# Optimization experiments

Measured on AMD Instinct MI355X. Metric: run time of the kernel, lower is better.

Reference implementation:

```python
import jax, jax.numpy as jnp
import numpy as np

B, T, M, C, H = 2, 2048, 512, 512, 8
D = C // H
SCALE = 1.0 / np.sqrt(D).astype(np.float32)


def _linear_params(key, din, dout):
    kw, kb = jax.random.split(key)
    W = jax.random.normal(kw, (din, dout), jnp.float32) * 0.02
    b = jax.random.normal(kb, (dout,), jnp.float32) * 0.02
    return W, b


def setup_inputs() -> dict:
    key = jax.random.key(0)
    ks = jax.random.split(key, 8)
    x = jax.random.normal(ks[0], (B, T, C), jnp.float32)
    y = jax.random.normal(ks[1], (B, M, C), jnp.float32)
    # causal mask over the x (self / product-attn) axis, broadcasts to [B,H,T,T]
    attn_x_mask = jnp.tril(jnp.ones((T, T), jnp.int32))[None, None]
    Wqkv_x, bqkv_x = _linear_params(ks[2], C, 3 * C)
    Wqkv_y, bqkv_y = _linear_params(ks[3], C, 3 * C)
    Wgs, bgs = _linear_params(ks[4], C, C)
    Wgc, bgc = _linear_params(ks[5], C, C)
    Wp, bp = _linear_params(ks[6], C, C)
    return dict(x=x, y=y, attn_x_mask=attn_x_mask,
                Wqkv_x=Wqkv_x, bqkv_x=bqkv_x, Wqkv_y=Wqkv_y, bqkv_y=bqkv_y,
                Wgs=Wgs, bgs=bgs, Wgc=Wgc, bgc=bgc, Wp=Wp, bp=bp)


def _heads(t, L):
    # [B,L,C] -> [B,H,L,D]
    return t.reshape(B, L, H, D).transpose(0, 2, 1, 3)


def reference(x, y, attn_x_mask, Wqkv_x, bqkv_x, Wqkv_y, bqkv_y,
              Wgs, bgs, Wgc, bgc, Wp, bp):
    neg_inf = jnp.float32(-jnp.inf)
    qx, kx, vx = jnp.split(x @ Wqkv_x + bqkv_x, 3, axis=-1)
    qy, ky, vy = jnp.split(y @ Wqkv_y + bqkv_y, 3, axis=-1)
    q_x, k_x, v_x = _heads(qx, T), _heads(kx, T), _heads(vx, T)
    q_y, k_y, v_y = _heads(qy, M), _heads(ky, M), _heads(vy, M)

    # cross attention x -> y : [B,H,T,M]
    catt_x2y = jnp.einsum('bhtd,bhmd->bhtm', q_x, k_y) * SCALE
    cval_x2y = jnp.einsum('bhtm,bhmd->bhtd', jax.nn.softmax(catt_x2y, axis=-1), v_y)
    cval_x2y = cval_x2y.transpose(0, 2, 1, 3).reshape(B, T, C)

    # product attention: (x->y scores) @ (y->x scores) : [B,H,T,T]
    catt_y2x = jnp.einsum('bhmd,bhtd->bhmt', q_y, k_x) * SCALE
    prod = jnp.einsum('bhtm,bhms->bhts', catt_x2y, catt_y2x) * SCALE
    prod = jnp.where(attn_x_mask == 0, neg_inf, prod)
    cval_y2x = jnp.einsum('bhts,bhsd->bhtd', jax.nn.softmax(prod, axis=-1), v_x)
    cval_y2x = cval_y2x.transpose(0, 2, 1, 3).reshape(B, T, C)

    cval = cval_x2y + cval_y2x

    # self attention on x : [B,H,T,T]
    satt = jnp.einsum('bhtd,bhsd->bhts', q_x, k_x) * SCALE
    satt = jnp.where(attn_x_mask == 0, neg_inf, satt)
    sval = jnp.einsum('bhts,bhsd->bhtd', jax.nn.softmax(satt, axis=-1), v_x)
    sval = sval.transpose(0, 2, 1, 3).reshape(B, T, C)

    sgate = jax.nn.sigmoid(sval @ Wgs + bgs)
    cgate = jax.nn.sigmoid(cval @ Wgc + bgc)
    out = (sgate * cval + cgate * sval) @ Wp + bp
    return out
```

## Files before the change

### kernel.cpp

```cpp
#include <hip/hip_runtime.h>
#include <hip/hip_bf16.h>

typedef unsigned short ushort_t;
typedef __attribute__((ext_vector_type(8))) short s8v;
typedef __attribute__((ext_vector_type(4))) float f4;
typedef __attribute__((ext_vector_type(4))) unsigned short u16x4;

#define BB 2
#define TT 2048
#define MMM 512
#define CC 512
#define HH 8
#define DD 64
#define SCALE 0.125f
#define SCALE_L2E 0.18033688011112042f

__device__ __forceinline__ ushort_t f2bf(float v) {
    __hip_bfloat16 h = __float2bfloat16(v);
    return *reinterpret_cast<ushort_t*>(&h);
}
__device__ __forceinline__ float bf2f(ushort_t u) {
    __hip_bfloat16 h;
    *reinterpret_cast<ushort_t*>(&h) = u;
    return __bfloat162float(h);
}
__device__ __forceinline__ float exp2_raw(float v) {
    float p;
    asm("v_exp_f32 %0, %1" : "=v"(p) : "v"(v));
    return p;
}

__device__ __forceinline__ void gload16(const void* g, void* l) {
    __builtin_amdgcn_global_load_lds((const __attribute__((address_space(1))) void*)g,
                                     (__attribute__((address_space(3))) void*)l, 16, 0, 0);
}

__device__ __forceinline__ void transp32(const float* W, ushort_t* WT, int K, int N,
                                         int bx, int by, int tid) {
    const int k0 = by * 32, n0 = bx * 32;
    __shared__ float t[32][33];
    for (int i = tid; i < 1024; i += 256) {
        int r = i >> 5, c = i & 31;
        t[r][c] = W[(long)(k0 + r) * N + n0 + c];
    }
    __syncthreads();
    for (int i = tid; i < 1024; i += 256) {
        int r = i >> 5, c = i & 31;
        WT[(long)(n0 + r) * K + k0 + c] = f2bf(t[c][r]);
    }
}
__device__ __forceinline__ void cvt4(const float* s, ushort_t* d, long blk, int tid) {
    long i = (blk * 256 + tid) * 4;
    float4 v = *(const float4*)(s + i);
    u16x4 o;
    o[0] = f2bf(v.x); o[1] = f2bf(v.y); o[2] = f2bf(v.z); o[3] = f2bf(v.w);
    *(u16x4*)(d + i) = o;
}

__global__ __launch_bounds__(256) void prep_k(
    const float* __restrict__ x, const float* __restrict__ y,
    const float* __restrict__ Wqx, const float* __restrict__ Wqy,
    const float* __restrict__ Wgs, const float* __restrict__ Wgc,
    const float* __restrict__ Wp,
    ushort_t* __restrict__ xb, ushort_t* __restrict__ yb,
    ushort_t* __restrict__ WqxT, ushort_t* __restrict__ WqyT,
    ushort_t* __restrict__ WgsT, ushort_t* __restrict__ WgcT,
    ushort_t* __restrict__ WpT)
{
    const int bid = blockIdx.x, tid = threadIdx.x;
    if (bid < 2048)      cvt4(x, xb, bid, tid);
    else if (bid < 2560) cvt4(y, yb, bid - 2048, tid);
    else if (bid < 3328) { int l = bid - 2560; transp32(Wqx, WqxT, 512, 1536, l % 48, l / 48, tid); }
    else if (bid < 4096) { int l = bid - 3328; transp32(Wqy, WqyT, 512, 1536, l % 48, l / 48, tid); }
    else if (bid < 4352) { int l = bid - 4096; transp32(Wgs, WgsT, 512, 512, l % 16, l / 16, tid); }
    else if (bid < 4608) { int l = bid - 4352; transp32(Wgc, WgcT, 512, 512, l % 16, l / 16, tid); }
    else                 { int l = bid - 4608; transp32(Wp, WpT, 512, 512, l % 16, l / 16, tid); }
}

__global__ __launch_bounds__(256) void vT_fused(
    const ushort_t* __restrict__ qkvx, const ushort_t* __restrict__ qkvy,
    ushort_t* __restrict__ vxT, ushort_t* __restrict__ vyT,
    ushort_t* __restrict__ kyT, ushort_t* __restrict__ qyT)
{
    const int bx = blockIdx.x, z = blockIdx.y, b = z >> 3, h = z & 7;
    const ushort_t* src; ushort_t* dst; int S, s0; long sB, dZ;
    if (bx < 32)      { src = qkvx + 1024; dst = vxT; S = TT;  sB = (long)TT * 1536;  dZ = (long)64 * TT;  s0 = bx * 64; }
    else if (bx < 40) { src = qkvy + 1024; dst = vyT; S = MMM; sB = (long)MMM * 1536; dZ = (long)64 * MMM; s0 = (bx - 32) * 64; }
    else if (bx < 48) { src = qkvy + 512;  dst = kyT; S = MMM; sB = (long)MMM * 1536; dZ = (long)64 * MMM; s0 = (bx - 40) * 64; }
    else              { src = qkvy;        dst = qyT; S = MMM; sB = (long)MMM * 1536; dZ = (long)64 * MMM; s0 = (bx - 48) * 64; }
    const ushort_t* sp = src + (long)b * sB + (long)h * 64;
    ushort_t* dp = dst + (long)z * dZ;
    __shared__ __align__(16) ushort_t t[64][80];
    const int tid = threadIdx.x;
#pragma unroll
    for (int p = 0; p < 2; ++p) {
        int id = tid + p * 256;
        int r = id >> 3, cc = (id & 7) * 8;
        int cs = cc ^ ((r >> 3) * 8);
        *(s8v*)&t[r][cs] = *(const s8v*)&sp[(long)(s0 + r) * 1536 + cc];
    }
    __syncthreads();
#pragma unroll
    for (int p = 0; p < 2; ++p) {
        int id = tid + p * 256;
        int d = id >> 3, cc = (id & 7) * 8;
        s8v o;
#pragma unroll
        for (int k = 0; k < 8; ++k) {
            int r = cc + k;
            o[k] = (short)t[r][d ^ ((r >> 3) * 8)];
        }
        *(s8v*)&dp[(long)d * S + s0 + cc] = o;
    }
}

__device__ __forceinline__ void stage_rows128(const ushort_t* src, long k0,
                                              ushort_t* dstL, int w, int lane) {
#pragma unroll
    for (int n = 0; n < 4; ++n) {
        int f = w * 4096 + n * 1024 + lane * 16;
        int row = f >> 7;
        int blk_g = ((f & 127) >> 4) ^ (row & 7);
        gload16(src + (long)row * 512 + k0 + blk_g * 8, dstL + ((w * 4096 + n * 1024) >> 1));
    }
}
__device__ __forceinline__ void stage_rows64(const ushort_t* src, long k0,
                                             ushort_t* dstL, int w, int lane) {
#pragma unroll
    for (int n = 0; n < 2; ++n) {
        int f = w * 2048 + n * 1024 + lane * 16;
        int row = f >> 7;
        int blk_g = ((f & 127) >> 4) ^ (row & 7);
        gload16(src + (long)row * 512 + k0 + blk_g * 8, dstL + ((w * 2048 + n * 1024) >> 1));
    }
}

__global__ __launch_bounds__(256) void qkv_k(
    const ushort_t* __restrict__ xb, const ushort_t* __restrict__ yb,
    const ushort_t* __restrict__ WqxT, const ushort_t* __restrict__ WqyT,
    const float* __restrict__ bqx, const float* __restrict__ bqy,
    ushort_t* __restrict__ qkvx, ushort_t* __restrict__ qkvy)
{
    const int by = blockIdx.y;
    const ushort_t* A; const ushort_t* Bm; const float* bias; ushort_t* O;
    int r0, qcols;
    if (by < 32) { A = xb; Bm = WqxT; bias = bqx; O = qkvx; r0 = by * 128; qcols = 512; }
    else         { A = yb; Bm = WqyT; bias = bqy; O = qkvy; r0 = (by - 32) * 128; qcols = 0; }
    const int c0 = blockIdx.x * 128;
    const int tid = threadIdx.x, w = tid >> 6, lane = tid & 63;
    const int quad = lane >> 4, l15 = lane & 15;
    const int rowBase = (w >> 1) * 64, colBase = (w & 1) * 64;

    __shared__ __align__(16) ushort_t Al[2][128 * 64];
    __shared__ __align__(16) ushort_t Bl[2][128 * 64];

    const ushort_t* Ab = A + (long)r0 * 512;
    const ushort_t* Bb = Bm + (long)c0 * 512;

    f4 acc[4][4] = {};

    stage_rows128(Ab, 0, Al[0], w, lane);
    stage_rows128(Bb, 0, Bl[0], w, lane);
    __syncthreads();

    for (int kk = 0; kk < 8; ++kk) {
        const int cur = kk & 1;
        if (kk < 7) {
            stage_rows128(Ab, (kk + 1) * 64, Al[cur ^ 1], w, lane);
            stage_rows128(Bb, (kk + 1) * 64, Bl[cur ^ 1], w, lane);
        }
#pragma unroll
        for (int ks = 0; ks < 2; ++ks) {
            s8v af[4], bfr[4];
#pragma unroll
            for (int i = 0; i < 4; ++i) {
                int row = rowBase + 16 * i + l15;
                af[i] = *(const s8v*)&Al[cur][row * 64 + (((ks * 4 + quad) ^ (row & 7)) * 8)];
                int col = colBase + 16 * i + l15;
                bfr[i] = *(const s8v*)&Bl[cur][col * 64 + (((ks * 4 + quad) ^ (col & 7)) * 8)];
            }
#pragma unroll
            for (int i = 0; i < 4; ++i)
#pragma unroll
                for (int j = 0; j < 4; ++j)
                    acc[i][j] = __builtin_amdgcn_mfma_f32_16x16x32_bf16(af[i], bfr[j], acc[i][j], 0, 0, 0);
        }
        __syncthreads();
    }

#pragma unroll
    for (int i = 0; i < 4; ++i)
#pragma unroll
        for (int j = 0; j < 4; ++j)
#pragma unroll
            for (int r = 0; r < 4; ++r) {
                int row = r0 + rowBase + 16 * i + quad * 4 + r;
                int col = c0 + colBase + 16 * j + l15;
                float v = acc[i][j][r] + bias[col];
                if (col < qcols) v *= SCALE_L2E;
                O[(long)row * 1536 + col] = f2bf(v);
            }
}

__global__ __launch_bounds__(256) void proj_k(
    const ushort_t* __restrict__ A, const ushort_t* __restrict__ Bm,
    float* __restrict__ O, const float* __restrict__ bias)
{
    const int r0 = blockIdx.y * 64, c0 = blockIdx.x * 64;
    const int tid = threadIdx.x, w = tid >> 6, lane = tid & 63;
    const int quad = lane >> 4, l15 = lane & 15;
    const int rowBase = (w >> 1) * 32, colBase = (w & 1) * 32;

    __shared__ __align__(16) ushort_t Al[3][64 * 64];
    __shared__ __align__(16) ushort_t Bl[3][64 * 64];

    const ushort_t* Ab = A + (long)r0 * 512;
    const ushort_t* Bb = Bm + (long)c0 * 512;

    f4 acc[2][2] = {};

    stage_rows64(Ab, 0, Al[0], w, lane);
    stage_rows64(Bb, 0, Bl[0], w, lane);
    stage_rows64(Ab, 64, Al[1], w, lane);
    stage_rows64(Bb, 64, Bl[1], w, lane);

    int cur = 0;
    for (int kk = 0; kk < 8; ++kk) {
        if (kk + 1 < 8) asm volatile("s_waitcnt vmcnt(4)" ::: "memory");
        else            asm volatile("s_waitcnt vmcnt(0)" ::: "memory");
        asm volatile("s_barrier" ::: "memory");
        if (kk + 2 < 8) {
            int s = cur + 2; if (s >= 3) s -= 3;
            stage_rows64(Ab, (kk + 2) * 64, Al[s], w, lane);
            stage_rows64(Bb, (kk + 2) * 64, Bl[s], w, lane);
        }
#pragma unroll
        for (int ks = 0; ks < 2; ++ks) {
            s8v af[2], bfr[2];
#pragma unroll
            for (int i = 0; i < 2; ++i) {
                int row = rowBase + 16 * i + l15;
                af[i] = *(const s8v*)&Al[cur][row * 64 + (((ks * 4 + quad) ^ (row & 7)) * 8)];
                int col = colBase + 16 * i + l15;
                bfr[i] = *(const s8v*)&Bl[cur][col * 64 + (((ks * 4 + quad) ^ (col & 7)) * 8)];
            }
#pragma unroll
            for (int i = 0; i < 2; ++i)
#pragma unroll
                for (int j = 0; j < 2; ++j)
                    acc[i][j] = __builtin_amdgcn_mfma_f32_16x16x32_bf16(af[i], bfr[j], acc[i][j], 0, 0, 0);
        }
        if (++cur == 3) cur = 0;
    }

#pragma unroll
    for (int i = 0; i < 2; ++i)
#pragma unroll
        for (int j = 0; j < 2; ++j)
#pragma unroll
            for (int r = 0; r < 4; ++r) {
                int row = r0 + rowBase + 16 * i + quad * 4 + r;
                int col = c0 + colBase + 16 * j + l15;
                O[(long)row * 512 + col] = acc[i][j][r] + bias[col];
            }
}

__global__ __launch_bounds__(256) void gt_k(const ushort_t* __restrict__ qyT,
                                            const ushort_t* __restrict__ kyT,
                                            ushort_t* __restrict__ Gt)
{
    const int z = blockIdx.x;
    const int tid = threadIdx.x, w = tid >> 6, lane = tid & 63;
    const int quad = lane >> 4, l15 = lane & 15;
    const ushort_t* A  = qyT + (long)z * 64 * MMM;
    const ushort_t* Bm = kyT + (long)z * 64 * MMM;
    __shared__ float red[4][4096];
    f4 acc[4][4] = {};
    for (int kk = 0; kk < 4; ++kk) {
        const int ks = w * 4 + kk;
        s8v af[4], bfr[4];
#pragma unroll
        for (int i = 0; i < 4; ++i) {
            af[i]  = *(const s8v*)(A  + (long)(16 * i + l15) * MMM + ks * 32 + quad * 8);
            bfr[i] = *(const s8v*)(Bm + (long)(16 * i + l15) * MMM + ks * 32 + quad * 8);
        }
#pragma unroll
        for (int i = 0; i < 4; ++i)
#pragma unroll
            for (int j = 0; j < 4; ++j)
                acc[i][j] = __builtin_amdgcn_mfma_f32_16x16x32_bf16(af[i], bfr[j], acc[i][j], 0, 0, 0);
    }
#pragma unroll
    for (int i = 0; i < 4; ++i)
#pragma unroll
        for (int j = 0; j < 4; ++j)
            *(f4*)&red[w][(i * 4 + j) * 256 + lane * 4] = acc[i][j];
    __syncthreads();
    const float s2 = SCALE * SCALE;
#pragma unroll
    for (int j = 0; j < 4; ++j) {
        f4 s = *(const f4*)&red[0][(w * 4 + j) * 256 + lane * 4];
#pragma unroll
        for (int ww = 1; ww < 4; ++ww)
            s += *(const f4*)&red[ww][(w * 4 + j) * 256 + lane * 4];
#pragma unroll
        for (int r = 0; r < 4; ++r) {
            int d2 = 16 * w + quad * 4 + r, d1 = 16 * j + l15;
            Gt[(long)z * 4096 + d2 * 64 + d1] = f2bf(s2 * s[r]);
        }
    }
}

__device__ __forceinline__ void stage_k64(const ushort_t* src, long rstride, int s0,
                                          ushort_t* Kl, int w, int lane) {
#pragma unroll
    for (int n = 0; n < 2; ++n) {
        int f = w * 2048 + n * 1024 + lane * 16;
        int row = f >> 7;
        int krow = ((row & 15) << 2) | (row >> 4);
        int blk = ((f & 127) >> 4) ^ (row & 7);
        gload16(src + (long)(s0 + krow) * rstride + blk * 8, &Kl[(w * 2048 + n * 1024) >> 1]);
    }
}
__device__ __forceinline__ void stage_v64(const ushort_t* src, long rstride, int s0,
                                          ushort_t* Vl, int w, int lane) {
#pragma unroll
    for (int n = 0; n < 2; ++n) {
        int f = w * 2048 + n * 1024 + lane * 16;
        int row = f >> 7;
        int blk = ((f & 127) >> 4) ^ (row & 7);
        gload16(src + (long)row * rstride + s0 + blk * 8, &Vl[(w * 2048 + n * 1024) >> 1]);
    }
}
__device__ __forceinline__ void qk8(f4 Sc[4], const s8v qf[2], const ushort_t* Kl,
                                    int quad, int l15) {
    __builtin_amdgcn_s_setprio(1);
#pragma unroll
    for (int ks = 0; ks < 2; ++ks)
#pragma unroll
        for (int c = 0; c < 4; ++c) {
            int row = 16 * c + l15;
            s8v bb = *(const s8v*)&Kl[row * 64 + (((ks * 4 + quad) ^ (row & 7)) * 8)];
            Sc[c] = __builtin_amdgcn_mfma_f32_16x16x32_bf16(qf[ks], bb, Sc[c], 0, 0, 0);
        }
    __builtin_amdgcn_s_setprio(0);
}
__device__ __forceinline__ void qk8_dual(f4 Ss[4], f4 Sp[4], const s8v qa[2], const s8v qb[2],
                                         const ushort_t* Kl, int quad, int l15) {
    __builtin_amdgcn_s_setprio(1);
#pragma unroll
    for (int ks = 0; ks < 2; ++ks)
#pragma unroll
        for (int c = 0; c < 4; ++c) {
            int row = 16 * c + l15;
            s8v bb = *(const s8v*)&Kl[row * 64 + (((ks * 4 + quad) ^ (row & 7)) * 8)];
            Ss[c] = __builtin_amdgcn_mfma_f32_16x16x32_bf16(qa[ks], bb, Ss[c], 0, 0, 0);
            Sp[c] = __builtin_amdgcn_mfma_f32_16x16x32_bf16(qb[ks], bb, Sp[c], 0, 0, 0);
        }
    __builtin_amdgcn_s_setprio(0);
}
__device__ __forceinline__ void vload8(s8v vf[8], const ushort_t* Vl, int quad, int l15) {
#pragma unroll
    for (int ks = 0; ks < 2; ++ks)
#pragma unroll
        for (int c = 0; c < 4; ++c) {
            int row = 16 * c + l15;
            vf[ks * 4 + c] = *(const s8v*)&Vl[row * 64 + (((ks * 4 + quad) ^ (row & 7)) * 8)];
        }
}
__device__ __forceinline__ void smax0(const f4 Sc[4], float l_i[4], ushort_t* PlW,
                                      int diag, int trow0, int s0, int quad, int l15) {
#pragma unroll
    for (int r = 0; r < 4; ++r) {
        const int trow = trow0 + quad * 4 + r;
        u16x4 o;
#pragma unroll
        for (int c = 0; c < 4; ++c) {
            float v = Sc[c][r];
            if (diag && (s0 + 4 * l15 + c) > trow) v = -3e38f;
            float p = exp2_raw(v);
            l_i[r] += p;
            o[c] = f2bf(p);
        }
        *(u16x4*)&PlW[(quad * 4 + r) * 72 + 4 * l15] = o;
    }
}
__device__ __forceinline__ void pv8r(f4 Oc[4], const ushort_t* PlW, const s8v vf[8],
                                     int quad, int l15) {
    __builtin_amdgcn_s_setprio(1);
#pragma unroll
    for (int ks = 0; ks < 2; ++ks) {
        s8v a = *(const s8v*)&PlW[l15 * 72 + ks * 32 + quad * 8];
#pragma unroll
        for (int c = 0; c < 4; ++c)
            Oc[c] = __builtin_amdgcn_mfma_f32_16x16x32_bf16(a, vf[ks * 4 + c], Oc[c], 0, 0, 0);
    }
    __builtin_amdgcn_s_setprio(0);
}
__device__ __forceinline__ void pv8r_dual(f4 Os[4], f4 Op[4], const ushort_t* Ps,
                                          const ushort_t* Pp, const s8v vf[8],
                                          int quad, int l15) {
    __builtin_amdgcn_s_setprio(1);
#pragma unroll
    for (int ks = 0; ks < 2; ++ks) {
        s8v as = *(const s8v*)&Ps[l15 * 72 + ks * 32 + quad * 8];
        s8v ap = *(const s8v*)&Pp[l15 * 72 + ks * 32 + quad * 8];
#pragma unroll
        for (int c = 0; c < 4; ++c) {
            Os[c] = __builtin_amdgcn_mfma_f32_16x16x32_bf16(as, vf[ks * 4 + c], Os[c], 0, 0, 0);
            Op[c] = __builtin_amdgcn_mfma_f32_16x16x32_bf16(ap, vf[ks * 4 + c], Op[c], 0, 0, 0);
        }
    }
    __builtin_amdgcn_s_setprio(0);
}

__global__ __launch_bounds__(256, 2) void flash_fused(
    const ushort_t* __restrict__ qkvx, const ushort_t* __restrict__ qkvy,
    const ushort_t* __restrict__ Gt, const ushort_t* __restrict__ vxT,
    const ushort_t* __restrict__ vyT,
    ushort_t* __restrict__ cval, ushort_t* __restrict__ sval)
{
    const int z = blockIdx.y, b = z >> 3, h = z & 7;
    const ushort_t* qx = qkvx + (long)b * (TT * 1536) + h * 64;
    const ushort_t* kx = qx + 512;
    const ushort_t* ky = qkvy + (long)b * (MMM * 1536) + 512 + h * 64;
    const ushort_t* Gz = Gt + (long)z * 4096;
    const ushort_t* vx = vxT + (long)z * (64 * TT);
    const ushort_t* vy = vyT + (long)z * (64 * MMM);

    const int xw = (z & 8) ? (int)blockIdx.x : (int)(gridDim.x - 1 - blockIdx.x);
    const int t0 = xw * 64;
    const int tid = threadIdx.x, w = tid >> 6, lane = tid & 63;
    const int quad = lane >> 4, l15 = lane & 15;

    __shared__ __align__(16) ushort_t Kl[2][64 * 64];
    __shared__ __align__(16) ushort_t Vl[2][64 * 64];
    __shared__ __align__(16) ushort_t Pl[2][4 * 16 * 72];
    ushort_t* PlWs = &Pl[0][w * 1152];
    ushort_t* PlWp = &Pl[1][w * 1152];

    stage_k64(ky, 1536, 0, Kl[0], w, lane);
    stage_v64(vy, MMM, 0, Vl[0], w, lane);

    const int qrow = t0 + 16 * w + l15;
    s8v qfx[2], qft[2];
    qfx[0] = *(const s8v*)(qx + (long)qrow * 1536 + quad * 8);
    qfx[1] = *(const s8v*)(qx + (long)qrow * 1536 + 32 + quad * 8);
    {
        f4 qa[4] = {};
#pragma unroll
        for (int ks = 0; ks < 2; ++ks)
#pragma unroll
            for (int j = 0; j < 4; ++j) {
                s8v bb = *(const s8v*)(Gz + (4 * l15 + j) * 64 + ks * 32 + quad * 8);
                qa[j] = __builtin_amdgcn_mfma_f32_16x16x32_bf16(qfx[ks], bb, qa[j], 0, 0, 0);
            }
#pragma unroll
        for (int r = 0; r < 4; ++r) {
            u16x4 o;
#pragma unroll
            for (int j = 0; j < 4; ++j) o[j] = f2bf(qa[j][r]);
            *(u16x4*)&PlWs[(quad * 4 + r) * 72 + 4 * l15] = o;
        }
        qft[0] = *(const s8v*)&PlWs[l15 * 72 + quad * 8];
        qft[1] = *(const s8v*)&PlWs[l15 * 72 + 32 + quad * 8];
    }

    f4 Occ[4] = {}, Ocs[4] = {}, Ocp[4] = {};
    float lc[4] = {}, ls[4] = {}, lp[4] = {};

    const int nT1 = MMM / 64;
    const int nTiles = nT1 + t0 / 64 + 1;

    for (int ti = 0; ti < nTiles; ++ti) {
        const int bi = ti & 1;
        __syncthreads();
        if (ti + 1 < nTiles) {
            const int tn = ti + 1, bn = tn & 1;
            if (tn < nT1) {
                stage_k64(ky, 1536, tn * 64, Kl[bn], w, lane);
                stage_v64(vy, MMM, tn * 64, Vl[bn], w, lane);
            } else {
                const int s0n = (tn - nT1) * 64;
                stage_k64(kx, 1536, s0n, Kl[bn], w, lane);
                stage_v64(vx, TT, s0n, Vl[bn], w, lane);
            }
        }
        if (ti < nT1) {
            f4 Sc[4] = {};
            qk8(Sc, qfx, Kl[bi], quad, l15);
            s8v vf[8];
            vload8(vf, Vl[bi], quad, l15);
            smax0(Sc, lc, PlWs, 0, 0, 0, quad, l15);
            pv8r(Occ, PlWs, vf, quad, l15);
        } else {
            const int s0 = (ti - nT1) * 64;
            const int diag = (s0 == t0);
            f4 Ss[4] = {}, Sp[4] = {};
            qk8_dual(Ss, Sp, qfx, qft, Kl[bi], quad, l15);
            s8v vf[8];
            vload8(vf, Vl[bi], quad, l15);
            smax0(Ss, ls, PlWs, diag, t0 + 16 * w, s0, quad, l15);
            smax0(Sp, lp, PlWp, diag, t0 + 16 * w, s0, quad, l15);
            pv8r_dual(Ocs, Ocp, PlWs, PlWp, vf, quad, l15);
        }
    }

#pragma unroll
    for (int r = 0; r < 4; ++r)
#pragma unroll
        for (int mb = 1; mb < 16; mb <<= 1) {
            lc[r] += __shfl_xor(lc[r], mb, 64);
            ls[r] += __shfl_xor(ls[r], mb, 64);
            lp[r] += __shfl_xor(lp[r], mb, 64);
        }

    const long ob = (long)b * (TT * CC) + h * 64;
#pragma unroll
    for (int r = 0; r < 4; ++r) {
        int row = t0 + 16 * w + quad * 4 + r;
        float ic = 1.f / lc[r], ip = 1.f / lp[r], isv = 1.f / ls[r];
#pragma unroll
        for (int c = 0; c < 4; ++c) {
            long idx = ob + (long)row * CC + 16 * c + l15;
            cval[idx] = f2bf(Occ[c][r] * ic + Ocp[c][r] * ip);
            sval[idx] = f2bf(Ocs[c][r] * isv);
        }
    }
}

__global__ __launch_bounds__(256) void gate_gemm(
    const ushort_t* __restrict__ sval, const ushort_t* __restrict__ cvalb,
    const ushort_t* __restrict__ WgsT, const ushort_t* __restrict__ WgcT,
    const float* __restrict__ bgs, const float* __restrict__ bgc,
    ushort_t* __restrict__ tmpb)
{
    const int r0 = blockIdx.y * 64, c0 = blockIdx.x * 64;
    const int tid = threadIdx.x, w = tid >> 6, lane = tid & 63;
    const int quad = lane >> 4, l15 = lane & 15;
    const int rowBase = (w >> 1) * 32, colBase = (w & 1) * 32;

    __shared__ __align__(16) ushort_t Al[3][64 * 64];
    __shared__ __align__(16) ushort_t Bl[3][64 * 64];

    const ushort_t* Ap[2] = { sval + (long)r0 * 512, cvalb + (long)r0 * 512 };
    const ushort_t* Bp[2] = { WgsT + (long)c0 * 512, WgcT + (long)c0 * 512 };

    f4 acc1[2][2] = {}, acc2[2][2] = {};

    stage_rows64(Ap[0], 0, Al[0], w, lane);
    stage_rows64(Bp[0], 0, Bl[0], w, lane);
    stage_rows64(Ap[0], 64, Al[1], w, lane);
    stage_rows64(Bp[0], 64, Bl[1], w, lane);

    int cur = 0;
    for (int st = 0; st < 16; ++st) {
        if (st + 1 < 16) asm volatile("s_waitcnt vmcnt(4)" ::: "memory");
        else             asm volatile("s_waitcnt vmcnt(0)" ::: "memory");
        asm volatile("s_barrier" ::: "memory");
        if (st + 2 < 16) {
            int s = cur + 2; if (s >= 3) s -= 3;
            const int nx = st + 2, p = nx >> 3;
            stage_rows64(Ap[p], (nx & 7) * 64, Al[s], w, lane);
            stage_rows64(Bp[p], (nx & 7) * 64, Bl[s], w, lane);
        }
#pragma unroll
        for (int ks = 0; ks < 2; ++ks) {
            s8v af[2], bfr[2];
#pragma unroll
            for (int i = 0; i < 2; ++i) {
                int row = rowBase + 16 * i + l15;
                af[i] = *(const s8v*)&Al[cur][row * 64 + (((ks * 4 + quad) ^ (row & 7)) * 8)];
                int col = colBase + 16 * i + l15;
                bfr[i] = *(const s8v*)&Bl[cur][col * 64 + (((ks * 4 + quad) ^ (col & 7)) * 8)];
            }
            if (st < 8) {
#pragma unroll
                for (int i = 0; i < 2; ++i)
#pragma unroll
                    for (int j = 0; j < 2; ++j)
                        acc1[i][j] = __builtin_amdgcn_mfma_f32_16x16x32_bf16(af[i], bfr[j], acc1[i][j], 0, 0, 0);
            } else {
#pragma unroll
                for (int i = 0; i < 2; ++i)
#pragma unroll
                    for (int j = 0; j < 2; ++j)
                        acc2[i][j] = __builtin_amdgcn_mfma_f32_16x16x32_bf16(af[i], bfr[j], acc2[i][j], 0, 0, 0);
            }
        }
        if (++cur == 3) cur = 0;
    }

#pragma unroll
    for (int i = 0; i < 2; ++i)
#pragma unroll
        for (int j = 0; j < 2; ++j)
#pragma unroll
            for (int r = 0; r < 4; ++r) {
                int row = r0 + rowBase + 16 * i + quad * 4 + r;
                int col = c0 + colBase + 16 * j + l15;
                long idx = (long)row * 512 + col;
                float g1 = 1.f / (1.f + __expf(-(acc1[i][j][r] + bgs[col])));
                float g2 = 1.f / (1.f + __expf(-(acc2[i][j][r] + bgc[col])));
                tmpb[idx] = f2bf(g1 * bf2f(cvalb[idx]) + g2 * bf2f(sval[idx]));
            }
}

extern "C" void kernel_launch(void* const* d_in, const int* in_sizes, int n_in,
                              void* d_out, int out_size, void* d_ws, size_t ws_size,
                              hipStream_t stream) {
    const float* x      = (const float*)d_in[0];
    const float* y      = (const float*)d_in[1];
    const float* Wqkv_x = (const float*)d_in[3];
    const float* bqkv_x = (const float*)d_in[4];
    const float* Wqkv_y = (const float*)d_in[5];
    const float* bqkv_y = (const float*)d_in[6];
    const float* Wgs    = (const float*)d_in[7];
    const float* bgs    = (const float*)d_in[8];
    const float* Wgc    = (const float*)d_in[9];
    const float* bgc    = (const float*)d_in[10];
    const float* Wp     = (const float*)d_in[11];
    const float* bp     = (const float*)d_in[12];
    float* out = (float*)d_out;

    ushort_t* u = (ushort_t*)d_ws;
    long o = 0;
    ushort_t* xb    = u + o; o += (long)BB * TT * CC;
    ushort_t* yb    = u + o; o += (long)BB * MMM * CC;
    ushort_t* WqxT  = u + o; o += 1536L * 512;
    ushort_t* WqyT  = u + o; o += 1536L * 512;
    ushort_t* WgsT  = u + o; o += 512L * 512;
    ushort_t* WgcT  = u + o; o += 512L * 512;
    ushort_t* WpT   = u + o; o += 512L * 512;
    ushort_t* qkvx  = u + o; o += (long)BB * TT * 1536;
    ushort_t* qkvy  = u + o; o += (long)BB * MMM * 1536;
    ushort_t* vxT   = u + o; o += (long)BB * HH * DD * TT;
    ushort_t* vyT   = u + o; o += (long)BB * HH * DD * MMM;
    ushort_t* kyT   = u + o; o += (long)BB * HH * DD * MMM;
    ushort_t* qyT   = u + o; o += (long)BB * HH * DD * MMM;
    ushort_t* Gt    = u + o; o += 16L * 64 * 64;
    ushort_t* cvalb = u + o; o += (long)BB * TT * CC;
    ushort_t* sval  = u + o; o += (long)BB * TT * CC;
    ushort_t* tmpb  = u + o; o += (long)BB * TT * CC;

    dim3 blk(256);

    prep_k<<<dim3(4864), blk, 0, stream>>>(x, y, Wqkv_x, Wqkv_y, Wgs, Wgc, Wp,
                                           xb, yb, WqxT, WqyT, WgsT, WgcT, WpT);

    qkv_k<<<dim3(12, 40), blk, 0, stream>>>(xb, yb, WqxT, WqyT, bqkv_x, bqkv_y, qkvx, qkvy);

    vT_fused<<<dim3(56, 16), blk, 0, stream>>>(qkvx, qkvy, vxT, vyT, kyT, qyT);

    gt_k<<<dim3(16), blk, 0, stream>>>(qyT, kyT, Gt);

    flash_fused<<<dim3(32, 16), blk, 0, stream>>>(qkvx, qkvy, Gt, vxT, vyT, cvalb, sval);

    gate_gemm<<<dim3(8, 64), blk, 0, stream>>>(sval, cvalb, WgsT, WgcT, bgs, bgc, tmpb);

    proj_k<<<dim3(8, 64), blk, 0, stream>>>(tmpb, WpT, out, bp);
}
```

Measured before the change: 205.8 us.

## Keep softmax probabilities in registers by computing transposed scores in flash kernel

Swaps the MFMA operands in the QK step so each lane holds a score column whose layout matches the A-operand of a 16x16x16 bf16 MFMA. The P@V product then uses the probabilities directly from registers, which removes the per-wave LDS round trip for P and the Pl shared buffer. V is read in 4-element chunks to match the new layout, the K staging row permutation is dropped, and row sums are reduced and broadcast with shuffles. The trade-off is twice as many smaller MFMAs for P@V, and correctness now depends on the new masking index math and the Kl[1] scratch reuse.

Result: no change. 209.2 us (+1.7%).

```diff
diff --git a/kernel.cpp b/kernel.cpp
--- a/kernel.cpp
+++ b/kernel.cpp
@@ -3,6 +3,7 @@
 
 typedef unsigned short ushort_t;
 typedef __attribute__((ext_vector_type(8))) short s8v;
+typedef __attribute__((ext_vector_type(4))) short s4v;
 typedef __attribute__((ext_vector_type(4))) float f4;
 typedef __attribute__((ext_vector_type(4))) unsigned short u16x4;
 
@@ -28,6 +29,21 @@
     float p;
     asm("v_exp_f32 %0, %1" : "=v"(p) : "v"(v));
     return p;
+}
+
+#if defined(__has_builtin)
+#if __has_builtin(__builtin_amdgcn_mfma_f32_16x16x16bf16_1k)
+#define HAVE_MFMA16 1
+#endif
+#endif
+__device__ __forceinline__ f4 mfma16(s4v a, s4v b, f4 c) {
+#ifdef HAVE_MFMA16
+    return __builtin_amdgcn_mfma_f32_16x16x16bf16_1k(a, b, c, 0, 0, 0);
+#else
+    s8v a8 = {a[0], a[1], a[2], a[3], 0, 0, 0, 0};
+    s8v b8 = {b[0], b[1], b[2], b[3], 0, 0, 0, 0};
+    return __builtin_amdgcn_mfma_f32_16x16x32_bf16(a8, b8, c, 0, 0, 0);
+#endif
 }
 
 __device__ __forceinline__ void gload16(const void* g, void* l) {
@@ -317,9 +333,8 @@
     for (int n = 0; n < 2; ++n) {
         int f = w * 2048 + n * 1024 + lane * 16;
         int row = f >> 7;
-        int krow = ((row & 15) << 2) | (row >> 4);
         int blk = ((f & 127) >> 4) ^ (row & 7);
-        gload16(src + (long)(s0 + krow) * rstride + blk * 8, &Kl[(w * 2048 + n * 1024) >> 1]);
+        gload16(src + (long)(s0 + row) * rstride + blk * 8, &Kl[(w * 2048 + n * 1024) >> 1]);
     }
 }
 __device__ __forceinline__ void stage_v64(const ushort_t* src, long rstride, int s0,
@@ -332,85 +347,78 @@
         gload16(src + (long)row * rstride + s0 + blk * 8, &Vl[(w * 2048 + n * 1024) >> 1]);
     }
 }
-__device__ __forceinline__ void qk8(f4 Sc[4], const s8v qf[2], const ushort_t* Kl,
-                                    int quad, int l15) {
+__device__ __forceinline__ void qk8_sw(f4 Sc[4], const s8v qf[2], const ushort_t* Kl,
+                                       int quad, int l15) {
     __builtin_amdgcn_s_setprio(1);
 #pragma unroll
     for (int ks = 0; ks < 2; ++ks)
 #pragma unroll
         for (int c = 0; c < 4; ++c) {
             int row = 16 * c + l15;
-            s8v bb = *(const s8v*)&Kl[row * 64 + (((ks * 4 + quad) ^ (row & 7)) * 8)];
-            Sc[c] = __builtin_amdgcn_mfma_f32_16x16x32_bf16(qf[ks], bb, Sc[c], 0, 0, 0);
+            s8v kk = *(const s8v*)&Kl[row * 64 + (((ks * 4 + quad) ^ (row & 7)) * 8)];
+            Sc[c] = __builtin_amdgcn_mfma_f32_16x16x32_bf16(kk, qf[ks], Sc[c], 0, 0, 0);
         }
     __builtin_amdgcn_s_setprio(0);
 }
-__device__ __forceinline__ void qk8_dual(f4 Ss[4], f4 Sp[4], const s8v qa[2], const s8v qb[2],
-                                         const ushort_t* Kl, int quad, int l15) {
+__device__ __forceinline__ void qk8_dual_sw(f4 Ss[4], f4 Sp[4], const s8v qa[2], const s8v qb[2],
+                                            const ushort_t* Kl, int quad, int l15) {
     __builtin_amdgcn_s_setprio(1);
 #pragma unroll
     for (int ks = 0; ks < 2; ++ks)
 #pragma unroll
         for (int c = 0; c < 4; ++c) {
             int row = 16 * c + l15;
-            s8v bb = *(const s8v*)&Kl[row * 64 + (((ks * 4 + quad) ^ (row & 7)) * 8)];
-            Ss[c] = __builtin_amdgcn_mfma_f32_16x16x32_bf16(qa[ks], bb, Ss[c], 0, 0, 0);
-            Sp[c] = __builtin_amdgcn_mfma_f32_16x16x32_bf16(qb[ks], bb, Sp[c], 0, 0, 0);
+            s8v kk = *(const s8v*)&Kl[row * 64 + (((ks * 4 + quad) ^ (row & 7)) * 8)];
+            Ss[c] = __builtin_amdgcn_mfma_f32_16x16x32_bf16(kk, qa[ks], Ss[c], 0, 0, 0);
+            Sp[c] = __builtin_amdgcn_mfma_f32_16x16x32_bf16(kk, qb[ks], Sp[c], 0, 0, 0);
         }
     __builtin_amdgcn_s_setprio(0);
 }
-__device__ __forceinline__ void vload8(s8v vf[8], const ushort_t* Vl, int quad, int l15) {
-#pragma unroll
-    for (int ks = 0; ks < 2; ++ks)
-#pragma unroll
-        for (int c = 0; c < 4; ++c) {
-            int row = 16 * c + l15;
-            vf[ks * 4 + c] = *(const s8v*)&Vl[row * 64 + (((ks * 4 + quad) ^ (row & 7)) * 8)];
-        }
-}
-__device__ __forceinline__ void smax0(const f4 Sc[4], float l_i[4], ushort_t* PlW,
-                                      int diag, int trow0, int s0, int quad, int l15) {
-#pragma unroll
-    for (int r = 0; r < 4; ++r) {
-        const int trow = trow0 + quad * 4 + r;
-        u16x4 o;
-#pragma unroll
-        for (int c = 0; c < 4; ++c) {
+__device__ __forceinline__ void vload16(s4v vb[16], const ushort_t* Vl, int quad, int l15) {
+#pragma unroll
+    for (int c = 0; c < 4; ++c)
+#pragma unroll
+        for (int td = 0; td < 4; ++td) {
+            int row = 16 * td + l15;
+            int blk = (2 * c + (quad >> 1)) ^ (row & 7);
+            vb[c * 4 + td] = *(const s4v*)&Vl[row * 64 + blk * 8 + (quad & 1) * 4];
+        }
+}
+__device__ __forceinline__ void smax_pack(const f4 Sc[4], float& l_acc, s4v pa[4],
+                                          int diag, int trow, int s0, int quad) {
+#pragma unroll
+    for (int c = 0; c < 4; ++c) {
+        s4v o;
+#pragma unroll
+        for (int r = 0; r < 4; ++r) {
             float v = Sc[c][r];
-            if (diag && (s0 + 4 * l15 + c) > trow) v = -3e38f;
+            if (diag && (s0 + 16 * c + 4 * quad + r) > trow) v = -3e38f;
             float p = exp2_raw(v);
-            l_i[r] += p;
-            o[c] = f2bf(p);
-        }
-        *(u16x4*)&PlW[(quad * 4 + r) * 72 + 4 * l15] = o;
-    }
-}
-__device__ __forceinline__ void pv8r(f4 Oc[4], const ushort_t* PlW, const s8v vf[8],
-                                     int quad, int l15) {
+            l_acc += p;
+            o[r] = (short)f2bf(p);
+        }
+        pa[c] = o;
+    }
+}
+__device__ __forceinline__ void pv16(f4 Oc[4], const s4v pa[4], const s4v vb[16]) {
     __builtin_amdgcn_s_setprio(1);
 #pragma unroll
-    for (int ks = 0; ks < 2; ++ks) {
-        s8v a = *(const s8v*)&PlW[l15 * 72 + ks * 32 + quad * 8];
-#pragma unroll
-        for (int c = 0; c < 4; ++c)
-            Oc[c] = __builtin_amdgcn_mfma_f32_16x16x32_bf16(a, vf[ks * 4 + c], Oc[c], 0, 0, 0);
-    }
+    for (int c = 0; c < 4; ++c)
+#pragma unroll
+        for (int td = 0; td < 4; ++td)
+            Oc[td] = mfma16(pa[c], vb[c * 4 + td], Oc[td]);
     __builtin_amdgcn_s_setprio(0);
 }
-__device__ __forceinline__ void pv8r_dual(f4 Os[4], f4 Op[4], const ushort_t* Ps,
-                                          const ushort_t* Pp, const s8v vf[8],
-                                          int quad, int l15) {
+__device__ __forceinline__ void pv16_dual(f4 Os[4], f4 Op[4], const s4v pas[4],
+                                          const s4v pap[4], const s4v vb[16]) {
     __builtin_amdgcn_s_setprio(1);
 #pragma unroll
-    for (int ks = 0; ks < 2; ++ks) {
-        s8v as = *(const s8v*)&Ps[l15 * 72 + ks * 32 + quad * 8];
-        s8v ap = *(const s8v*)&Pp[l15 * 72 + ks * 32 + quad * 8];
-#pragma unroll
-        for (int c = 0; c < 4; ++c) {
-            Os[c] = __builtin_amdgcn_mfma_f32_16x16x32_bf16(as, vf[ks * 4 + c], Os[c], 0, 0, 0);
-            Op[c] = __builtin_amdgcn_mfma_f32_16x16x32_bf16(ap, vf[ks * 4 + c], Op[c], 0, 0, 0);
-        }
-    }
+    for (int c = 0; c < 4; ++c)
+#pragma unroll
+        for (int td = 0; td < 4; ++td) {
+            Os[td] = mfma16(pas[c], vb[c * 4 + td], Os[td]);
+            Op[td] = mfma16(pap[c], vb[c * 4 + td], Op[td]);
+        }
     __builtin_amdgcn_s_setprio(0);
 }
 
@@ -432,12 +440,10 @@
     const int t0 = xw * 64;
     const int tid = threadIdx.x, w = tid >> 6, lane = tid & 63;
     const int quad = lane >> 4, l15 = lane & 15;
+    const int trow = t0 + 16 * w + l15;
 
     __shared__ __align__(16) ushort_t Kl[2][64 * 64];
     __shared__ __align__(16) ushort_t Vl[2][64 * 64];
-    __shared__ __align__(16) ushort_t Pl[2][4 * 16 * 72];
-    ushort_t* PlWs = &Pl[0][w * 1152];
-    ushort_t* PlWp = &Pl[1][w * 1152];
 
     stage_k64(ky, 1536, 0, Kl[0], w, lane);
     stage_v64(vy, MMM, 0, Vl[0], w, lane);
@@ -455,19 +461,20 @@
                 s8v bb = *(const s8v*)(Gz + (4 * l15 + j) * 64 + ks * 32 + quad * 8);
                 qa[j] = __builtin_amdgcn_mfma_f32_16x16x32_bf16(qfx[ks], bb, qa[j], 0, 0, 0);
             }
+        ushort_t* scr = &Kl[1][w * 1024];
 #pragma unroll
         for (int r = 0; r < 4; ++r) {
             u16x4 o;
 #pragma unroll
             for (int j = 0; j < 4; ++j) o[j] = f2bf(qa[j][r]);
-            *(u16x4*)&PlWs[(quad * 4 + r) * 72 + 4 * l15] = o;
-        }
-        qft[0] = *(const s8v*)&PlWs[l15 * 72 + quad * 8];
-        qft[1] = *(const s8v*)&PlWs[l15 * 72 + 32 + quad * 8];
+            *(u16x4*)&scr[(quad * 4 + r) * 64 + 4 * l15] = o;
+        }
+        qft[0] = *(const s8v*)&scr[l15 * 64 + quad * 8];
+        qft[1] = *(const s8v*)&scr[l15 * 64 + 32 + quad * 8];
     }
 
     f4 Occ[4] = {}, Ocs[4] = {}, Ocp[4] = {};
-    float lc[4] = {}, ls[4] = {}, lp[4] = {};
+    float lc = 0.f, ls = 0.f, lp = 0.f;
 
     const int nT1 = MMM / 64;
     const int nTiles = nT1 + t0 / 64 + 1;
@@ -488,43 +495,42 @@
         }
         if (ti < nT1) {
             f4 Sc[4] = {};
-            qk8(Sc, qfx, Kl[bi], quad, l15);
-            s8v vf[8];
-            vload8(vf, Vl[bi], quad, l15);
-            smax0(Sc, lc, PlWs, 0, 0, 0, quad, l15);
-            pv8r(Occ, PlWs, vf, quad, l15);
+            qk8_sw(Sc, qfx, Kl[bi], quad, l15);
+            s4v vb[16];
+            vload16(vb, Vl[bi], quad, l15);
+            s4v pa[4];
+            smax_pack(Sc, lc, pa, 0, 0, 0, quad);
+            pv16(Occ, pa, vb);
         } else {
             const int s0 = (ti - nT1) * 64;
             const int diag = (s0 == t0);
             f4 Ss[4] = {}, Sp[4] = {};
-            qk8_dual(Ss, Sp, qfx, qft, Kl[bi], quad, l15);
-            s8v vf[8];
-            vload8(vf, Vl[bi], quad, l15);
-            smax0(Ss, ls, PlWs, diag, t0 + 16 * w, s0, quad, l15);
-            smax0(Sp, lp, PlWp, diag, t0 + 16 * w, s0, quad, l15);
-            pv8r_dual(Ocs, Ocp, PlWs, PlWp, vf, quad, l15);
-        }
-    }
-
-#pragma unroll
-    for (int r = 0; r < 4; ++r)
-#pragma unroll
-        for (int mb = 1; mb < 16; mb <<= 1) {
-            lc[r] += __shfl_xor(lc[r], mb, 64);
-            ls[r] += __shfl_xor(ls[r], mb, 64);
-            lp[r] += __shfl_xor(lp[r], mb, 64);
-        }
+            qk8_dual_sw(Ss, Sp, qfx, qft, Kl[bi], quad, l15);
+            s4v vb[16];
+            vload16(vb, Vl[bi], quad, l15);
+            s4v pas[4], pap[4];
+            smax_pack(Ss, ls, pas, diag, trow, s0, quad);
+            smax_pack(Sp, lp, pap, diag, trow, s0, quad);
+            pv16_dual(Ocs, Ocp, pas, pap, vb);
+        }
+    }
+
+    lc += __shfl_xor(lc, 16, 64); lc += __shfl_xor(lc, 32, 64);
+    ls += __shfl_xor(ls, 16, 64); ls += __shfl_xor(ls, 32, 64);
+    lp += __shfl_xor(lp, 16, 64); lp += __shfl_xor(lp, 32, 64);
 
     const long ob = (long)b * (TT * CC) + h * 64;
 #pragma unroll
     for (int r = 0; r < 4; ++r) {
         int row = t0 + 16 * w + quad * 4 + r;
-        float ic = 1.f / lc[r], ip = 1.f / lp[r], isv = 1.f / ls[r];
-#pragma unroll
-        for (int c = 0; c < 4; ++c) {
-            long idx = ob + (long)row * CC + 16 * c + l15;
-            cval[idx] = f2bf(Occ[c][r] * ic + Ocp[c][r] * ip);
-            sval[idx] = f2bf(Ocs[c][r] * isv);
+        float ic  = 1.f / __shfl(lc, 4 * quad + r, 64);
+        float isv = 1.f / __shfl(ls, 4 * quad + r, 64);
+        float ip  = 1.f / __shfl(lp, 4 * quad + r, 64);
+#pragma unroll
+        for (int td = 0; td < 4; ++td) {
+            long idx = ob + (long)row * CC + 16 * td + l15;
+            cval[idx] = f2bf(Occ[td][r] * ic + Ocp[td][r] * ip);
+            sval[idx] = f2bf(Ocs[td][r] * isv);
         }
     }
 }
```
